# Kernel optimization log

Measured on AMD Instinct MI355X. Metric: run time of the kernel, lower is better.

## Reference

```python
import jax, jax.numpy as jnp
import numpy as np

NODE_NUM = 2048
DIM_IN = 2
DIM_OUT = 64
CHEB_K = 2
EMBED_DIM = 16
BATCH = 16


def _sagc(x, E, w_pool, b_pool):
    """AGCRN-style adaptive graph conv. x: [B,N,C]; E: [N,e];
    w_pool: [e,K,C,O]; b_pool: [e,O]. Returns (out [B,N,O], A [N,N])."""
    n = E.shape[0]
    A = E @ E.T                                   # [N,N] raw (signed) similarity
    supports = jax.nn.softmax(jax.nn.relu(A), axis=1)
    s_list = [jnp.eye(n, dtype=x.dtype), supports]
    for _ in range(2, CHEB_K):
        s_list.append(2.0 * supports @ s_list[-1] - s_list[-2])
    S = jnp.stack(s_list[:CHEB_K])                # [K,N,N]
    W = jnp.einsum('ne,ekio->nkio', E, w_pool)    # per-node weights [N,K,C,O]
    b = E @ b_pool                                # [N,O]
    x_g = jnp.einsum('knm,bmi->bnki', S, x)       # [B,N,K,C]
    out = jnp.einsum('bnki,nkio->bno', x_g, W) + b
    return out, A


def _degrees(adj_mask, H, weight):
    """adj_mask: [N,N] {0,1}; H: [B,N,D]; weight: [N,N] -> softmaxed [B,N,N]."""
    HHT = jnp.einsum('bnd,bmd->bnm', H, H)        # [B,N,N]
    AHHT = adj_mask * HHT                          # broadcast [N,N]*[B,N,N]
    AHHTW = jnp.einsum('bnm,mk->bnk', AHHT, weight)
    return jax.nn.softmax(AHHTW, axis=-1)


def setup_inputs() -> dict:
    key = jax.random.key(0)
    ks = jax.random.split(key, 9)
    din = DIM_IN + DIM_OUT
    return {
        'x': jax.random.normal(ks[0], (BATCH, NODE_NUM, DIM_IN), jnp.float32),
        'state': jax.random.normal(ks[1], (BATCH, NODE_NUM, DIM_OUT), jnp.float32),
        'node_embeddings': jax.random.normal(ks[2], (NODE_NUM, EMBED_DIM), jnp.float32) * 0.5,
        'weight_connect': jax.random.normal(ks[3], (NODE_NUM, NODE_NUM), jnp.float32) * 0.02,
        'weight_disconnect': jax.random.normal(ks[4], (NODE_NUM, NODE_NUM), jnp.float32) * 0.02,
        'gate_w': jax.random.normal(ks[5], (EMBED_DIM, CHEB_K, din, 2 * DIM_OUT), jnp.float32) * 0.05,
        'gate_b': jax.random.normal(ks[6], (EMBED_DIM, 2 * DIM_OUT), jnp.float32) * 0.05,
        'upd_w': jax.random.normal(ks[7], (EMBED_DIM, CHEB_K, din, DIM_OUT), jnp.float32) * 0.05,
        'upd_b': jax.random.normal(ks[8], (EMBED_DIM, DIM_OUT), jnp.float32) * 0.05,
    }


def reference(x, state, node_embeddings, weight_connect, weight_disconnect,
              gate_w, gate_b, upd_w, upd_b):
    inp = jnp.concatenate([x, state], axis=-1)            # [B,N,Cin+D]
    x_gconv, A = _sagc(inp, node_embeddings, gate_w, gate_b)
    z_r = jax.nn.sigmoid(x_gconv)
    z, r = jnp.split(z_r, 2, axis=-1)
    candidate = jnp.concatenate([x, z * state], axis=-1)
    hc = jnp.tanh(_sagc(candidate, node_embeddings, upd_w, upd_b)[0])
    h = r * state + (1.0 - r) * hc                        # [B,N,D]
    A_connect = jnp.where(A > 0, 1.0, 0.0).astype(h.dtype)
    A_disconnect = jnp.where(A < 0, 1.0, 0.0).astype(h.dtype)
    deg_c = _degrees(A_connect, h, weight_connect)        # [B,N,N]
    deg_d = _degrees(A_disconnect, h, weight_disconnect)
    numerator = (0.8 * h
                 - 0.1 * jnp.einsum('bnm,bmd->bnd', deg_c, h)
                 + 0.1 * jnp.einsum('bnm,bmd->bnd', deg_d, h))
    return numerator
```

## Files before the change

kernel.cpp:

```cpp
#include <hip/hip_runtime.h>
#include <hip/hip_bf16.h>

typedef unsigned short u16;
typedef unsigned int   u32;
typedef unsigned char  u8;

typedef __attribute__((ext_vector_type(8))) short bf16x8;
typedef __attribute__((ext_vector_type(4))) float f32x4;
typedef __attribute__((ext_vector_type(16))) float f32x16;

static __device__ __forceinline__ float bf2f(u16 u){ return __uint_as_float(((u32)u)<<16); }
static __device__ __forceinline__ u16 f2bf(float f){
  u32 u = __float_as_uint(f);
  u32 r = (u + 0x7fff + ((u>>16)&1)) >> 16;
  return (u16)r;
}

static __device__ __forceinline__ u8 f2fp8(float v){
  v = fminf(440.f, fmaxf(-440.f, v));
  return (u8)(__builtin_amdgcn_cvt_pk_fp8_f32(v, 0.f, 0, false) & 0xff);
}
static __device__ __forceinline__ u32 pk4_fp8(float a, float b, float c, float d){
  int w = __builtin_amdgcn_cvt_pk_fp8_f32(a, b, 0, false);
  w = __builtin_amdgcn_cvt_pk_fp8_f32(c, d, w, true);
  return (u32)w;
}

static __device__ __forceinline__ f32x4 mfma_bf16(bf16x8 a, bf16x8 b, f32x4 c){
  return __builtin_amdgcn_mfma_f32_16x16x32_bf16(a, b, c, 0, 0, 0);
}
static __device__ __forceinline__ f32x16 mfma_fp8_32(long a, long b, f32x16 c){
  return __builtin_amdgcn_mfma_f32_32x32x16_fp8_fp8(a, b, c, 0, 0, 0);
}
static __device__ __forceinline__ long lo64(uint4 v){ return (long)(((unsigned long long)v.y<<32) | v.x); }
static __device__ __forceinline__ long hi64(uint4 v){ return (long)(((unsigned long long)v.w<<32) | v.z); }
static __device__ __forceinline__ long mklong(u32 lo, u32 hi){ return (long)(((unsigned long long)hi<<32) | lo); }

__global__ void k_w8(const float* __restrict__ Wc, const float* __restrict__ Wd,
                     u8* __restrict__ Wc8, u8* __restrict__ Wd8){
  __shared__ float tile[64][65];
  const float* src = blockIdx.z ? Wd : Wc;
  u8* dst = blockIdx.z ? Wd8 : Wc8;
  const int m0 = blockIdx.x*64, k0 = blockIdx.y*64;
  const int t = threadIdx.x, r = t & 63, cc = t >> 6;
  #pragma unroll
  for (int j=0;j<4;j++){
    float4 v = *(const float4*)&src[(size_t)(m0+r)*2048 + k0 + cc*16 + j*4];
    tile[r][cc*16+j*4+0]=v.x; tile[r][cc*16+j*4+1]=v.y;
    tile[r][cc*16+j*4+2]=v.z; tile[r][cc*16+j*4+3]=v.w;
  }
  __syncthreads();
  const int lane = t & 63, sub = t >> 6;
  const int kth = sub & 1, mcp = sub >> 1;
  const int kl = kth*32 + (lane & 31);
  const int ml = mcp*32 + (lane >> 5)*8;
  u32 b0 = pk4_fp8(16.f*tile[ml+ 0][kl], 16.f*tile[ml+ 1][kl], 16.f*tile[ml+ 2][kl], 16.f*tile[ml+ 3][kl]);
  u32 b1 = pk4_fp8(16.f*tile[ml+ 4][kl], 16.f*tile[ml+ 5][kl], 16.f*tile[ml+ 6][kl], 16.f*tile[ml+ 7][kl]);
  u32 b2 = pk4_fp8(16.f*tile[ml+16][kl], 16.f*tile[ml+17][kl], 16.f*tile[ml+18][kl], 16.f*tile[ml+19][kl]);
  u32 b3 = pk4_fp8(16.f*tile[ml+20][kl], 16.f*tile[ml+21][kl], 16.f*tile[ml+22][kl], 16.f*tile[ml+23][kl]);
  const int pt = m0 >> 6, kt = (k0 >> 5) + kth;
  u8* dbase = dst + (size_t)((pt*64 + kt)*2 + mcp)*1024 + lane*16;
  *(uint4*)dbase = make_uint4(b0, b1, b2, b3);
}

__global__ void k_hcvt(const float* __restrict__ h, u16* __restrict__ hb16,
                       u8* __restrict__ ht8p, u16* __restrict__ hfm){
  __shared__ float tile[64][65];
  const int k0 = blockIdx.x*64, b = blockIdx.y;
  const int t = threadIdx.x, r = t & 63, cc = t >> 6;
  const float* src = h + ((size_t)b*2048 + k0)*64;
  u32 hw[8];
  #pragma unroll
  for (int j=0;j<4;j++){
    float4 v = *(const float4*)&src[(size_t)r*64 + cc*16 + j*4];
    tile[r][cc*16+j*4+0]=v.x; tile[r][cc*16+j*4+1]=v.y;
    tile[r][cc*16+j*4+2]=v.z; tile[r][cc*16+j*4+3]=v.w;
    hw[2*j]   = (u32)f2bf(v.x) | ((u32)f2bf(v.y)<<16);
    hw[2*j+1] = (u32)f2bf(v.z) | ((u32)f2bf(v.w)<<16);
  }
  u16* hp = hb16 + (((size_t)b*2048 + k0 + r)*64 + cc*16);
  *(uint4*)hp     = make_uint4(hw[0],hw[1],hw[2],hw[3]);
  *(uint4*)(hp+8) = make_uint4(hw[4],hw[5],hw[6],hw[7]);
  __syncthreads();
  {
    const int lane = t & 63, sub = cc;
    const int k16 = (k0 >> 4) + sub;
    const int lr = sub*16 + ((lane >> 5) << 3);
    const int d0 = lane & 31;
    #pragma unroll
    for (int dt=0; dt<2; ++dt){
      const int d = dt*32 + d0;
      u32 w0 = pk4_fp8(tile[lr+0][d], tile[lr+1][d], tile[lr+2][d], tile[lr+3][d]);
      u32 w1 = pk4_fp8(tile[lr+4][d], tile[lr+5][d], tile[lr+6][d], tile[lr+7][d]);
      *(uint2*)(ht8p + (size_t)b*131072 + (size_t)(k16*2 + dt)*512 + lane*8) = make_uint2(w0, w1);
    }
  }
  {
    const int col = k0 + r, ks = cc >> 1, q0 = (cc & 1)*2;
    const int ctg = col >> 4, lcv = col & 15;
    u16* fbase = hfm + (size_t)b*131072 + (size_t)ks*65536 + ((size_t)ctg*64)*8;
    #pragma unroll
    for (int qq=0; qq<2; ++qq){
      int q = q0 + qq;
      u32 p0 = (u32)f2bf(tile[r][ks*32+q*8+0]) | ((u32)f2bf(tile[r][ks*32+q*8+1])<<16);
      u32 p1 = (u32)f2bf(tile[r][ks*32+q*8+2]) | ((u32)f2bf(tile[r][ks*32+q*8+3])<<16);
      u32 p2 = (u32)f2bf(tile[r][ks*32+q*8+4]) | ((u32)f2bf(tile[r][ks*32+q*8+5])<<16);
      u32 p3 = (u32)f2bf(tile[r][ks*32+q*8+6]) | ((u32)f2bf(tile[r][ks*32+q*8+7])<<16);
      *(uint4*)(fbase + (size_t)(q*16 + lcv)*8) = make_uint4(p0,p1,p2,p3);
    }
  }
}

__global__ void k_P(const float* __restrict__ E, u16* __restrict__ P, u8* __restrict__ msk){
  __shared__ float Ew[16];
  __shared__ float arow[2048];
  __shared__ float red[4];
  const int t = threadIdx.x, n = blockIdx.x;
  if (t < 16) Ew[t] = E[n*16 + t];
  __syncthreads();
  float lmax = 0.f;
  for (int i=0;i<8;i++){
    int m = t + 256*i;
    const float* ep = E + m*16;
    float dot = 0.f;
    #pragma unroll
    for (int d=0; d<16; ++d) dot += Ew[d]*ep[d];
    msk[n*2048 + m] = dot > 0.f ? (u8)1 : (dot < 0.f ? (u8)2 : (u8)0);
    float ar = fmaxf(dot, 0.f);
    arow[m] = ar;
    lmax = fmaxf(lmax, ar);
  }
  for (int o=1;o<64;o<<=1) lmax = fmaxf(lmax, __shfl_xor(lmax, o));
  if ((t&63)==0) red[t>>6] = lmax;
  __syncthreads();
  float gmax = fmaxf(fmaxf(red[0],red[1]), fmaxf(red[2],red[3]));
  __syncthreads();
  float lsum = 0.f;
  for (int i=0;i<8;i++){
    int m = t + 256*i;
    float e = expf(arow[m] - gmax);
    arow[m] = e;
    lsum += e;
  }
  for (int o=1;o<64;o<<=1) lsum += __shfl_xor(lsum, o);
  if ((t&63)==0) red[t>>6] = lsum;
  __syncthreads();
  float inv = 1.f/(red[0]+red[1]+red[2]+red[3]);
  for (int i=0;i<8;i++){
    int m = t + 256*i;
    P[n*2048 + m] = f2bf(arow[m]*inv);
  }
}

__global__ void k_mbits(const u8* __restrict__ msk, u32* __restrict__ mp2, u32* __restrict__ mn2){
  const int m = blockIdx.x, nb = blockIdx.y*256;
  const int t = threadIdx.x, w = t>>6, lane = t&63;
  u8 v = msk[(size_t)(nb + t)*2048 + m];
  unsigned long long bp = __ballot(v == (u8)1);
  unsigned long long bn = __ballot(v == (u8)2);
  if (lane == 0){
    int wi = (nb + w*64) >> 5;
    mp2[(size_t)wi*2048 + m]     = (u32)bp;
    mp2[(size_t)(wi+1)*2048 + m] = (u32)(bp>>32);
    mn2[(size_t)wi*2048 + m]     = (u32)bn;
    mn2[(size_t)(wi+1)*2048 + m] = (u32)(bn>>32);
  }
}

__global__ void k_c1x(const u16* __restrict__ P, const float* __restrict__ x, float* __restrict__ c1x){
  const int t = threadIdx.x;
  const int r = t>>1, c = t&1;
  const int n = blockIdx.x*64 + r, b = blockIdx.y;
  const u16* pr = P + (size_t)n*2048;
  const float* xb = x + (size_t)b*2048*2 + c;
  float acc = 0.f;
  for (int m=0;m<2048;m+=4){
    acc += bf2f(pr[m+0])*xb[(m+0)*2];
    acc += bf2f(pr[m+1])*xb[(m+1)*2];
    acc += bf2f(pr[m+2])*xb[(m+2)*2];
    acc += bf2f(pr[m+3])*xb[(m+3)*2];
  }
  c1x[((size_t)b*2048 + n)*2 + c] = acc;
}

__global__ void k_conv(const u16* __restrict__ P, const float* __restrict__ Z, float* __restrict__ Y){
  __shared__ float Pt[16][68];
  __shared__ float Zt[16][68];
  const int t = threadIdx.x;
  const int tr = t>>4, tc = t&15;
  const int n0 = blockIdx.x*64, b = blockIdx.y;
  float acc[4][4] = {};
  for (int mt=0; mt<128; ++mt){
    int m0 = mt*16;
    {
      int r = t>>2, c4 = (t&3)*4;
      const u16* pp = P + (size_t)(n0+r)*2048 + m0 + c4;
      u32 p0 = *(const u32*)pp, p1v = *(const u32*)(pp+2);
      Pt[c4+0][r]=bf2f((u16)p0);  Pt[c4+1][r]=bf2f((u16)(p0>>16));
      Pt[c4+2][r]=bf2f((u16)p1v); Pt[c4+3][r]=bf2f((u16)(p1v>>16));
      int mm = t>>4, d0 = (t&15)*4;
      float4 zv = *(const float4*)&Z[((size_t)b*2048 + m0+mm)*64 + d0];
      Zt[mm][d0+0]=zv.x; Zt[mm][d0+1]=zv.y; Zt[mm][d0+2]=zv.z; Zt[mm][d0+3]=zv.w;
    }
    __syncthreads();
    #pragma unroll
    for (int mm=0; mm<16; ++mm){
      float4 a  = *(const float4*)&Pt[mm][tr*4];
      float4 bz = *(const float4*)&Zt[mm][tc*4];
      acc[0][0]+=a.x*bz.x; acc[0][1]+=a.x*bz.y; acc[0][2]+=a.x*bz.z; acc[0][3]+=a.x*bz.w;
      acc[1][0]+=a.y*bz.x; acc[1][1]+=a.y*bz.y; acc[1][2]+=a.y*bz.z; acc[1][3]+=a.y*bz.w;
      acc[2][0]+=a.z*bz.x; acc[2][1]+=a.z*bz.y; acc[2][2]+=a.z*bz.z; acc[2][3]+=a.z*bz.w;
      acc[3][0]+=a.w*bz.x; acc[3][1]+=a.w*bz.y; acc[3][2]+=a.w*bz.z; acc[3][3]+=a.w*bz.w;
    }
    __syncthreads();
  }
  #pragma unroll
  for (int i=0;i<4;i++){
    float4 v = make_float4(acc[i][0],acc[i][1],acc[i][2],acc[i][3]);
    *(float4*)&Y[((size_t)b*2048 + n0 + tr*4 + i)*64 + tc*4] = v;
  }
}

__global__ void k_gate(const float* __restrict__ E, const float* __restrict__ gw, const float* __restrict__ gb,
                       const float* __restrict__ x, const float* __restrict__ state,
                       const float* __restrict__ c1x, const float* __restrict__ c1s,
                       float* __restrict__ zs, float* __restrict__ rws){
  __shared__ float Ew[16];
  __shared__ float bnv[128];
  __shared__ float Wn[2][66][64];
  __shared__ float xg4[4][2][66];
  const int t = threadIdx.x, n = blockIdx.x;
  if (t < 16) Ew[t] = E[n*16 + t];
  __syncthreads();
  if (t < 128){
    float a = 0.f;
    #pragma unroll
    for (int e=0;e<16;e++) a += Ew[e]*gb[e*128 + t];
    bnv[t] = a;
  }
  for (int half=0; half<2; ++half){
    for (int idx=t; idx<8448; idx+=256){
      int o = idx & 63, rest = idx>>6, i = rest % 66, k = rest / 66;
      float a = 0.f;
      #pragma unroll
      for (int e=0;e<16;e++) a += Ew[e]*gw[((e*2+k)*66 + i)*128 + half*64 + o];
      Wn[k][i][o] = a;
    }
    __syncthreads();
    for (int bb=0; bb<4; ++bb){
      for (int idx=t; idx<528; idx+=256){
        int bi = idx/132, rem = idx%132, k = rem/66, i = rem%66;
        int b = bb*4 + bi;
        float v;
        if (k==0) v = (i<2) ? x[((size_t)b*2048+n)*2 + i] : state[((size_t)b*2048+n)*64 + (i-2)];
        else      v = (i<2) ? c1x[((size_t)b*2048+n)*2 + i] : c1s[((size_t)b*2048+n)*64 + (i-2)];
        xg4[bi][k][i] = v;
      }
      __syncthreads();
      {
        int bi = t>>6, o = t&63, b = bb*4 + bi;
        float a = 0.f;
        #pragma unroll
        for (int k=0;k<2;k++)
          for (int i=0;i<66;i++) a += xg4[bi][k][i]*Wn[k][i][o];
        a += bnv[half*64 + o];
        float s = 1.f/(1.f + expf(-a));
        if (half==0) zs[((size_t)b*2048+n)*64 + o] = s*state[((size_t)b*2048+n)*64 + o];
        else         rws[((size_t)b*2048+n)*64 + o] = s;
      }
      __syncthreads();
    }
  }
}

__global__ void k_upd(const float* __restrict__ E, const float* __restrict__ uw, const float* __restrict__ ub,
                      const float* __restrict__ x, const float* __restrict__ state,
                      const float* __restrict__ zs, const float* __restrict__ c1x, const float* __restrict__ c2s,
                      const float* __restrict__ rws, float* __restrict__ h){
  __shared__ float Ew[16];
  __shared__ float bnu[64];
  __shared__ float Wn[2][66][64];
  __shared__ float xg4[4][2][66];
  const int t = threadIdx.x, n = blockIdx.x;
  if (t < 16) Ew[t] = E[n*16 + t];
  __syncthreads();
  if (t < 64){
    float a = 0.f;
    #pragma unroll
    for (int e=0;e<16;e++) a += Ew[e]*ub[e*64 + t];
    bnu[t] = a;
  }
  for (int idx=t; idx<8448; idx+=256){
    int o = idx & 63, rest = idx>>6, i = rest % 66, k = rest / 66;
    float a = 0.f;
    #pragma unroll
    for (int e=0;e<16;e++) a += Ew[e]*uw[((e*2+k)*66 + i)*64 + o];
    Wn[k][i][o] = a;
  }
  __syncthreads();
  for (int bb=0; bb<4; ++bb){
    for (int idx=t; idx<528; idx+=256){
      int bi = idx/132, rem = idx%132, k = rem/66, i = rem%66;
      int b = bb*4 + bi;
      float v;
      if (k==0) v = (i<2) ? x[((size_t)b*2048+n)*2 + i] : zs[((size_t)b*2048+n)*64 + (i-2)];
      else      v = (i<2) ? c1x[((size_t)b*2048+n)*2 + i] : c2s[((size_t)b*2048+n)*64 + (i-2)];
      xg4[bi][k][i] = v;
    }
    __syncthreads();
    {
      int bi = t>>6, o = t&63, b = bb*4 + bi;
      float a = 0.f;
      #pragma unroll
      for (int k=0;k<2;k++)
        for (int i=0;i<66;i++) a += xg4[bi][k][i]*Wn[k][i][o];
      float hc = tanhf(a + bnu[o]);
      float rv = rws[((size_t)b*2048+n)*64 + o];
      h[((size_t)b*2048+n)*64 + o] = rv*state[((size_t)b*2048+n)*64 + o] + (1.f - rv)*hc;
    }
    __syncthreads();
  }
}

#define SROW8 2056

__global__ void __launch_bounds__(512,2) k_deg(
    const u32* __restrict__ mbits, const u16* __restrict__ hb16,
    const u8* __restrict__ W8,
    const u8* __restrict__ ht8p, const u16* __restrict__ hfm,
    const float* __restrict__ hf32, const float* __restrict__ oc_in,
    float* __restrict__ outp, int fin){
  extern __shared__ u8 S[];
  __shared__ float maxw[64][4];
  __shared__ float sumw[64][4];
  __shared__ float sgl_lds[64];
  const int t = threadIdx.x;
  const int w = t >> 6, lane = t & 63, lc = lane & 15, q = lane >> 4;
  const int l32 = lane & 31, h32 = lane >> 5;
  const int id = blockIdx.x;
  const int b = id >> 5, n0 = (id & 31) * 64;
  const int p0 = (id >> 3) & 31;
  const u32* mrow0 = mbits + (size_t)(n0 >> 5)*2048;
  const u32* mrow1 = mrow0 + 2048;
  const u16* hbb = hb16 + (size_t)b*2048*64;
  const u16* hfb = hfm + (size_t)b*131072;
  const u8* htb = ht8p + (size_t)b*131072;

  {
    const int c0 = p0 & 15;
    bf16x8 A[4][2];
    #pragma unroll
    for (int rt=0; rt<4; ++rt)
      #pragma unroll
      for (int ks=0; ks<2; ++ks)
        A[rt][ks] = *(const bf16x8*)&hbb[(size_t)(n0 + rt*16 + lc)*64 + ks*32 + q*8];
    int ctg0 = w*16 + c0;
    bf16x8 B0c = *(const bf16x8*)(hfb + (size_t)ctg0*512 + lane*8);
    bf16x8 B1c = *(const bf16x8*)(hfb + 65536 + (size_t)ctg0*512 + lane*8);
    u32 m0c = mrow0[ctg0*16 + lc], m1c = mrow1[ctg0*16 + lc];
    #pragma unroll 1
    for (int ct=0; ct<16; ++ct){
      const int ctg  = w*16 + ((ct + c0) & 15);
      const int ctgn = w*16 + ((ct + 1 + c0) & 15);
      bf16x8 B0n = *(const bf16x8*)(hfb + (size_t)ctgn*512 + lane*8);
      bf16x8 B1n = *(const bf16x8*)(hfb + 65536 + (size_t)ctgn*512 + lane*8);
      u32 m0n = mrow0[ctgn*16 + lc], m1n = mrow1[ctgn*16 + lc];
      const int mcol = ctg*16 + lc;
      f32x4 a[4];
      #pragma unroll
      for (int rt=0; rt<4; ++rt){
        a[rt] = (f32x4){0.f,0.f,0.f,0.f};
        a[rt] = mfma_bf16(A[rt][0], B0c, a[rt]);
        a[rt] = mfma_bf16(A[rt][1], B1c, a[rt]);
      }
      #pragma unroll
      for (int rt=0; rt<4; ++rt){
        const u32 mw = (rt < 2) ? m0c : m1c;
        #pragma unroll
        for (int i=0;i<4;i++){
          const int row = rt*16 + q*4 + i;
          float v = ((mw >> (row & 31)) & 1u) ? a[rt][i]*0.125f : 0.f;
          S[row*SROW8 + mcol] = f2fp8(v);
        }
      }
      B0c = B0n; B1c = B1n; m0c = m0n; m1c = m1n;
    }
  }
  __syncthreads();

  const int nh = w >> 2, kq = w & 3;
  const u8* sbase = S + (size_t)(nh*32 + l32)*SROW8 + h32*8;
  const u8* wl = W8 + lane*16;
  f32x16 o0 = (f32x16)(0.f), o1 = (f32x16)(0.f);
  float mrun = -1e30f, srun = 0.f;
  const float LN256 = 5.545177444479562f;
  #pragma unroll 1
  for (int si = 0; si < 4; ++si){
    const int ktb = kq*16 + si*4;
    f32x16 L[4];
    #pragma unroll
    for (int tt=0; tt<4; ++tt) L[tt] = (f32x16)(0.f);
    uint4 wv[8];
    {
      const int pt0 = p0 & 31;
      #pragma unroll
      for (int tt=0; tt<4; ++tt){
        wv[tt*2+0] = *(const uint4*)(wl + (size_t)(((pt0*64 + ktb+tt)*2 + 0))*1024);
        wv[tt*2+1] = *(const uint4*)(wl + (size_t)(((pt0*64 + ktb+tt)*2 + 1))*1024);
      }
    }
    __builtin_amdgcn_s_setprio(1);
    #pragma unroll 1
    for (int pti = 0; pti < 32; ++pti){
      const int pt  = (pti + p0) & 31;
      const int ptn = (pti + 1 + p0) & 31;
      long b0 = *(const long*)(sbase + pt*64 +  0);
      long b1 = *(const long*)(sbase + pt*64 + 16);
      long b2 = *(const long*)(sbase + pt*64 + 32);
      long b3 = *(const long*)(sbase + pt*64 + 48);
      uint4 wn[8];
      #pragma unroll
      for (int tt=0; tt<4; ++tt){
        wn[tt*2+0] = *(const uint4*)(wl + (size_t)(((ptn*64 + ktb+tt)*2 + 0))*1024);
        wn[tt*2+1] = *(const uint4*)(wl + (size_t)(((ptn*64 + ktb+tt)*2 + 1))*1024);
      }
      #pragma unroll
      for (int tt=0; tt<4; ++tt) L[tt] = mfma_fp8_32(lo64(wv[tt*2+0]), b0, L[tt]);
      #pragma unroll
      for (int tt=0; tt<4; ++tt) L[tt] = mfma_fp8_32(hi64(wv[tt*2+0]), b1, L[tt]);
      #pragma unroll
      for (int tt=0; tt<4; ++tt) L[tt] = mfma_fp8_32(lo64(wv[tt*2+1]), b2, L[tt]);
      #pragma unroll
      for (int tt=0; tt<4; ++tt) L[tt] = mfma_fp8_32(hi64(wv[tt*2+1]), b3, L[tt]);
      #pragma unroll
      for (int i=0; i<8; ++i) wv[i] = wn[i];
    }
    __builtin_amdgcn_s_setprio(0);
    float cmax = L[0][0];
    #pragma unroll
    for (int tt=0; tt<4; ++tt)
      #pragma unroll
      for (int g=0; g<16; ++g) cmax = fmaxf(cmax, L[tt][g]);
    cmax = fmaxf(cmax, __shfl_xor(cmax, 32));
    float mnew = fmaxf(mrun, 0.5f*cmax);
    float sc = __expf(mrun - mnew);
    srun *= sc;
    #pragma unroll
    for (int g=0; g<16; ++g){
      const int rowl = (g&3) + 8*(g>>2) + 4*h32;
      float fr = __shfl(sc, rowl);
      o0[g] *= fr; o1[g] *= fr;
    }
    float cs = 0.f;
    #pragma unroll
    for (int tt=0; tt<4; ++tt){
      float p[16];
      #pragma unroll
      for (int g=0; g<16; ++g){
        p[g] = __expf(0.5f*L[tt][g] - mnew + LN256);
        cs += p[g];
      }
      u32 qA = pk4_fp8(p[0],p[1],p[2],p[3]);
      u32 qB = pk4_fp8(p[4],p[5],p[6],p[7]);
      u32 qC = pk4_fp8(p[8],p[9],p[10],p[11]);
      u32 qD = pk4_fp8(p[12],p[13],p[14],p[15]);
      u32 xA = __shfl_xor(qA, 32), xB = __shfl_xor(qB, 32);
      u32 xC = __shfl_xor(qC, 32), xD = __shfl_xor(qD, 32);
      long pf0 = h32 ? mklong(xB, qB) : mklong(qA, xA);
      long pf1 = h32 ? mklong(xD, qD) : mklong(qC, xC);
      const int kt = ktb + tt;
      long h00 = *(const long*)(htb + (size_t)((kt*2+0)*2 + 0)*512 + lane*8);
      long h01 = *(const long*)(htb + (size_t)((kt*2+0)*2 + 1)*512 + lane*8);
      long h10 = *(const long*)(htb + (size_t)((kt*2+1)*2 + 0)*512 + lane*8);
      long h11 = *(const long*)(htb + (size_t)((kt*2+1)*2 + 1)*512 + lane*8);
      o0 = mfma_fp8_32(pf0, h00, o0);
      o1 = mfma_fp8_32(pf0, h01, o1);
      o0 = mfma_fp8_32(pf1, h10, o0);
      o1 = mfma_fp8_32(pf1, h11, o1);
    }
    cs += __shfl_xor(cs, 32);
    srun += cs;
    mrun = mnew;
  }

  if (lane < 32){
    maxw[nh*32 + lane][kq] = mrun;
    sumw[nh*32 + lane][kq] = srun;
  }
  __syncthreads();
  {
    float m_gl = maxw[nh*32 + l32][0];
    #pragma unroll
    for (int j=1;j<4;j++) m_gl = fmaxf(m_gl, maxw[nh*32 + l32][j]);
    float s_gl = 0.f;
    #pragma unroll
    for (int j=0;j<4;j++) s_gl += sumw[nh*32 + l32][j] * __expf(maxw[nh*32 + l32][j] - m_gl);
    if (kq == 0 && lane < 32) sgl_lds[nh*32 + lane] = s_gl;
    float f = __expf(mrun - m_gl);
    float* scr = (float*)S;
    #pragma unroll
    for (int g=0; g<16; ++g){
      const int rowl = (g&3) + 8*(g>>2) + 4*h32;
      float fr = __shfl(f, rowl);
      scr[(size_t)(kq*2 + nh)*2048 + (size_t)g*64 + lane]      = o0[g]*fr;
      scr[(size_t)(kq*2 + nh)*2048 + (size_t)(16+g)*64 + lane] = o1[g]*fr;
    }
  }
  __syncthreads();

  {
    const float* scr = (const float*)S;
    const int n_g = t >> 3, d0 = (t & 7)*8;
    const int nh_r = n_g >> 5, nl = n_g & 31;
    const int h32r = (nl >> 2) & 1;
    const int rr = nl - 4*h32r;
    const int g = (rr & 3) | ((rr >> 3) << 2);
    const float sdiv = sgl_lds[n_g];
    float* op = outp + (size_t)b*2048*64;
    const float* hp = hf32 + (size_t)b*2048*64;
    const float* cp = oc_in + (size_t)b*2048*64;
    #pragma unroll
    for (int j=0;j<8;j++){
      const int d = d0 + j;
      const int dt = d >> 5;
      const int lanei = (d & 31) + 32*h32r;
      float v = 0.f;
      #pragma unroll
      for (int kqr=0; kqr<4; ++kqr)
        v += scr[(size_t)(kqr*2 + nh_r)*2048 + (size_t)(dt*16 + g)*64 + lanei];
      v /= sdiv;
      size_t idx = (size_t)(n0 + n_g)*64 + d;
      if (fin) v = 0.8f*hp[idx] - 0.1f*cp[idx] + 0.1f*v;
      op[idx] = v;
    }
  }
}

extern "C" void kernel_launch(void* const* d_in, const int* in_sizes, int n_in,
                              void* d_out, int out_size, void* d_ws, size_t ws_size,
                              hipStream_t stream) {
  const float* x     = (const float*)d_in[0];
  const float* state = (const float*)d_in[1];
  const float* E     = (const float*)d_in[2];
  const float* Wc    = (const float*)d_in[3];
  const float* Wd    = (const float*)d_in[4];
  const float* gw    = (const float*)d_in[5];
  const float* gb    = (const float*)d_in[6];
  const float* uw    = (const float*)d_in[7];
  const float* ub    = (const float*)d_in[8];

  char* base = (char*)d_ws;
  u16*   P    = (u16*)(base + 0);
  u32*   mp2  = (u32*)(base + 0);
  u32*   mn2  = (u32*)(base + 524288);
  u8*    msk  = (u8*) (base + 8388608);
  u8*    Wc8  = (u8*) (base + 12582912);
  u8*    Wd8  = (u8*) (base + 16777216);
  u16*   hb16 = (u16*)(base + 20971520);
  u8*    ht8p = (u8*) (base + 25165824);
  u16*   hfm  = (u16*)(base + 27262976);
  float* c1x  = (float*)(base + 31457280);
  float* c1s  = (float*)(base + 31719424);
  float* zs   = (float*)(base + 40108032);
  float* rws  = (float*)(base + 48496640);
  float* c2s  = (float*)(base + 56885248);
  float* h    = (float*)(base + 65273856);
  float* oc   = c1s;
  float* od   = c2s;

  k_w8<<<dim3(32,32,2), 256, 0, stream>>>(Wc, Wd, Wc8, Wd8);
  k_P<<<2048, 256, 0, stream>>>(E, P, msk);
  k_c1x<<<dim3(32,16), 128, 0, stream>>>(P, x, c1x);
  k_conv<<<dim3(32,16), 256, 0, stream>>>(P, state, c1s);
  k_gate<<<2048, 256, 0, stream>>>(E, gw, gb, x, state, c1x, c1s, zs, rws);
  k_conv<<<dim3(32,16), 256, 0, stream>>>(P, zs, c2s);
  k_upd<<<2048, 256, 0, stream>>>(E, uw, ub, x, state, zs, c1x, c2s, rws, h);
  k_hcvt<<<dim3(32,16), 256, 0, stream>>>(h, hb16, ht8p, hfm);
  k_mbits<<<dim3(2048,8), 256, 0, stream>>>(msk, mp2, mn2);

  const int deg_lds = 64*SROW8;
  hipFuncSetAttribute((const void*)k_deg, hipFuncAttributeMaxDynamicSharedMemorySize, deg_lds);
  k_deg<<<512, 512, deg_lds, stream>>>(mp2, hb16, Wc8, ht8p, hfm, h, h, oc, 0);
  k_deg<<<512, 512, deg_lds, stream>>>(mn2, hb16, Wd8, ht8p, hfm, h, oc, (float*)d_out, 1);
}
```

Baseline: 1.232 ms.

## Use MFMA with split-bf16 in k_conv and repartition k_deg warps over K

k_conv now uses 32x32x16 bf16 MFMA instead of a scalar FP32 outer-product loop. It keeps accuracy by splitting Z into high and low bf16 parts and summing two accumulators. In k_deg, each of the 8 warps now covers both 32-row halves of the 64-node tile over its own K slice, instead of the old 2x4 node-half by K-quarter split. This lets each weight fragment loaded from global memory feed two MFMAs, halving W8 traffic per warp. The cost is more accumulator registers per warp and an 8-way reduction of softmax partials and outputs through LDS.

```diff
diff --git a/kernel.cpp b/kernel.cpp
--- a/kernel.cpp
+++ b/kernel.cpp
@@ -28,6 +28,9 @@
 
 static __device__ __forceinline__ f32x4 mfma_bf16(bf16x8 a, bf16x8 b, f32x4 c){
   return __builtin_amdgcn_mfma_f32_16x16x32_bf16(a, b, c, 0, 0, 0);
+}
+static __device__ __forceinline__ f32x16 mfma_bf16_32(bf16x8 a, bf16x8 b, f32x16 c){
+  return __builtin_amdgcn_mfma_f32_32x32x16_bf16(a, b, c, 0, 0, 0);
 }
 static __device__ __forceinline__ f32x16 mfma_fp8_32(long a, long b, f32x16 c){
   return __builtin_amdgcn_mfma_f32_32x32x16_fp8_fp8(a, b, c, 0, 0, 0);
@@ -184,40 +187,49 @@
 }
 
 __global__ void k_conv(const u16* __restrict__ P, const float* __restrict__ Z, float* __restrict__ Y){
-  __shared__ float Pt[16][68];
-  __shared__ float Zt[16][68];
+  __shared__ u16 Pt[64][68];
+  __shared__ u16 Zhi[64][68];
+  __shared__ u16 Zlo[64][68];
   const int t = threadIdx.x;
-  const int tr = t>>4, tc = t&15;
+  const int w = t >> 6, lane = t & 63, l32 = lane & 31, h32 = lane >> 5;
+  const int nh = w & 1, dh = w >> 1;
   const int n0 = blockIdx.x*64, b = blockIdx.y;
-  float acc[4][4] = {};
-  for (int mt=0; mt<128; ++mt){
-    int m0 = mt*16;
+  const int mloc = t & 63, grp = t >> 6;
+  f32x16 acch = (f32x16)(0.f), accl = (f32x16)(0.f);
+  for (int mc = 0; mc < 32; ++mc){
+    const int m0 = mc*64;
     {
-      int r = t>>2, c4 = (t&3)*4;
-      const u16* pp = P + (size_t)(n0+r)*2048 + m0 + c4;
-      u32 p0 = *(const u32*)pp, p1v = *(const u32*)(pp+2);
-      Pt[c4+0][r]=bf2f((u16)p0);  Pt[c4+1][r]=bf2f((u16)(p0>>16));
-      Pt[c4+2][r]=bf2f((u16)p1v); Pt[c4+3][r]=bf2f((u16)(p1v>>16));
-      int mm = t>>4, d0 = (t&15)*4;
-      float4 zv = *(const float4*)&Z[((size_t)b*2048 + m0+mm)*64 + d0];
-      Zt[mm][d0+0]=zv.x; Zt[mm][d0+1]=zv.y; Zt[mm][d0+2]=zv.z; Zt[mm][d0+3]=zv.w;
+      const u16* pp = P + (size_t)(n0 + mloc)*2048 + m0 + grp*16;
+      uint4 v0 = *(const uint4*)pp;
+      uint4 v1 = *(const uint4*)(pp + 8);
+      *(uint4*)&Pt[mloc][grp*16]     = v0;
+      *(uint4*)&Pt[mloc][grp*16 + 8] = v1;
+      const float* zp = Z + ((size_t)b*2048 + m0 + mloc)*64 + grp*16;
+      #pragma unroll
+      for (int jj = 0; jj < 4; ++jj){
+        float4 zv = *(const float4*)(zp + jj*4);
+        const int dd = grp*16 + jj*4;
+        u16 h0 = f2bf(zv.x); Zhi[dd+0][mloc] = h0; Zlo[dd+0][mloc] = f2bf(zv.x - bf2f(h0));
+        u16 h1 = f2bf(zv.y); Zhi[dd+1][mloc] = h1; Zlo[dd+1][mloc] = f2bf(zv.y - bf2f(h1));
+        u16 h2 = f2bf(zv.z); Zhi[dd+2][mloc] = h2; Zlo[dd+2][mloc] = f2bf(zv.z - bf2f(h2));
+        u16 h3 = f2bf(zv.w); Zhi[dd+3][mloc] = h3; Zlo[dd+3][mloc] = f2bf(zv.w - bf2f(h3));
+      }
     }
     __syncthreads();
     #pragma unroll
-    for (int mm=0; mm<16; ++mm){
-      float4 a  = *(const float4*)&Pt[mm][tr*4];
-      float4 bz = *(const float4*)&Zt[mm][tc*4];
-      acc[0][0]+=a.x*bz.x; acc[0][1]+=a.x*bz.y; acc[0][2]+=a.x*bz.z; acc[0][3]+=a.x*bz.w;
-      acc[1][0]+=a.y*bz.x; acc[1][1]+=a.y*bz.y; acc[1][2]+=a.y*bz.z; acc[1][3]+=a.y*bz.w;
-      acc[2][0]+=a.z*bz.x; acc[2][1]+=a.z*bz.y; acc[2][2]+=a.z*bz.z; acc[2][3]+=a.z*bz.w;
-      acc[3][0]+=a.w*bz.x; acc[3][1]+=a.w*bz.y; acc[3][2]+=a.w*bz.z; acc[3][3]+=a.w*bz.w;
+    for (int kt = 0; kt < 4; ++kt){
+      bf16x8 a  = *(const bf16x8*)&Pt[nh*32 + l32][kt*16 + h32*8];
+      bf16x8 bh = *(const bf16x8*)&Zhi[dh*32 + l32][kt*16 + h32*8];
+      bf16x8 bl = *(const bf16x8*)&Zlo[dh*32 + l32][kt*16 + h32*8];
+      acch = mfma_bf16_32(a, bh, acch);
+      accl = mfma_bf16_32(a, bl, accl);
     }
     __syncthreads();
   }
   #pragma unroll
-  for (int i=0;i<4;i++){
-    float4 v = make_float4(acc[i][0],acc[i][1],acc[i][2],acc[i][3]);
-    *(float4*)&Y[((size_t)b*2048 + n0 + tr*4 + i)*64 + tc*4] = v;
+  for (int g = 0; g < 16; ++g){
+    const int row = (g&3) + 8*(g>>2) + 4*h32;
+    Y[((size_t)b*2048 + n0 + nh*32 + row)*64 + dh*32 + l32] = acch[g] + accl[g];
   }
 }
 
@@ -322,6 +334,58 @@
   }
 }
 
+static __device__ __forceinline__ void sm_step(f32x16& LK0, f32x16& LK1,
+    f32x16& OA, f32x16& OB, float& mrun, float& srun,
+    const u8* __restrict__ htb, int ktA, int ktB, int lane, int h32){
+  const float LN256 = 5.545177444479562f;
+  float cmax = LK0[0];
+  #pragma unroll
+  for (int g=1; g<16; ++g) cmax = fmaxf(cmax, LK0[g]);
+  #pragma unroll
+  for (int g=0; g<16; ++g) cmax = fmaxf(cmax, LK1[g]);
+  cmax = fmaxf(cmax, __shfl_xor(cmax, 32));
+  float mnew = fmaxf(mrun, 0.5f*cmax);
+  float sc = __expf(mrun - mnew);
+  srun *= sc;
+  #pragma unroll
+  for (int g=0; g<16; ++g){
+    const int rowl = (g&3) + 8*(g>>2) + 4*h32;
+    float fr = __shfl(sc, rowl);
+    OA[g] *= fr; OB[g] *= fr;
+  }
+  float cs = 0.f;
+  #pragma unroll
+  for (int kti=0; kti<2; ++kti){
+    const int kt = kti ? ktB : ktA;
+    float p[16];
+    #pragma unroll
+    for (int g=0; g<16; ++g){
+      float Lg = kti ? LK1[g] : LK0[g];
+      p[g] = __expf(0.5f*Lg - mnew + LN256);
+      cs += p[g];
+    }
+    u32 qA = pk4_fp8(p[0],p[1],p[2],p[3]);
+    u32 qB = pk4_fp8(p[4],p[5],p[6],p[7]);
+    u32 qC = pk4_fp8(p[8],p[9],p[10],p[11]);
+    u32 qD = pk4_fp8(p[12],p[13],p[14],p[15]);
+    u32 xA = __shfl_xor(qA,32), xB = __shfl_xor(qB,32);
+    u32 xC = __shfl_xor(qC,32), xD = __shfl_xor(qD,32);
+    long pf0 = h32 ? mklong(xB,qB) : mklong(qA,xA);
+    long pf1 = h32 ? mklong(xD,qD) : mklong(qC,xC);
+    long h00 = *(const long*)(htb + (size_t)((kt*2+0)*2 + 0)*512 + lane*8);
+    long h01 = *(const long*)(htb + (size_t)((kt*2+0)*2 + 1)*512 + lane*8);
+    long h10 = *(const long*)(htb + (size_t)((kt*2+1)*2 + 0)*512 + lane*8);
+    long h11 = *(const long*)(htb + (size_t)((kt*2+1)*2 + 1)*512 + lane*8);
+    OA = mfma_fp8_32(pf0, h00, OA);
+    OB = mfma_fp8_32(pf0, h01, OB);
+    OA = mfma_fp8_32(pf1, h10, OA);
+    OB = mfma_fp8_32(pf1, h11, OB);
+  }
+  cs += __shfl_xor(cs, 32);
+  srun += cs;
+  mrun = mnew;
+}
+
 #define SROW8 2056
 
 __global__ void __launch_bounds__(512,2) k_deg(
@@ -331,8 +395,8 @@
     const float* __restrict__ hf32, const float* __restrict__ oc_in,
     float* __restrict__ outp, int fin){
   extern __shared__ u8 S[];
-  __shared__ float maxw[64][4];
-  __shared__ float sumw[64][4];
+  __shared__ float maxw[64][8];
+  __shared__ float sumw[64][8];
   __shared__ float sgl_lds[64];
   const int t = threadIdx.x;
   const int w = t >> 6, lane = t & 63, lc = lane & 15, q = lane >> 4;
@@ -388,133 +452,105 @@
   }
   __syncthreads();
 
-  const int nh = w >> 2, kq = w & 3;
-  const u8* sbase = S + (size_t)(nh*32 + l32)*SROW8 + h32*8;
+  const u8* sb0 = S + (size_t)l32*SROW8 + h32*8;
+  const u8* sb1 = S + (size_t)(32 + l32)*SROW8 + h32*8;
   const u8* wl = W8 + lane*16;
-  f32x16 o0 = (f32x16)(0.f), o1 = (f32x16)(0.f);
-  float mrun = -1e30f, srun = 0.f;
-  const float LN256 = 5.545177444479562f;
+  f32x16 oA0 = (f32x16)(0.f), oA1 = (f32x16)(0.f);
+  f32x16 oB0 = (f32x16)(0.f), oB1 = (f32x16)(0.f);
+  float mrun0 = -1e30f, srun0 = 0.f, mrun1 = -1e30f, srun1 = 0.f;
   #pragma unroll 1
   for (int si = 0; si < 4; ++si){
-    const int ktb = kq*16 + si*4;
-    f32x16 L[4];
-    #pragma unroll
-    for (int tt=0; tt<4; ++tt) L[tt] = (f32x16)(0.f);
-    uint4 wv[8];
+    const int ktA = w*8 + si*2, ktB = ktA + 1;
+    f32x16 L00 = (f32x16)(0.f), L01 = (f32x16)(0.f);
+    f32x16 L10 = (f32x16)(0.f), L11 = (f32x16)(0.f);
+    uint4 wv0, wv1, wv2, wv3;
     {
-      const int pt0 = p0 & 31;
-      #pragma unroll
-      for (int tt=0; tt<4; ++tt){
-        wv[tt*2+0] = *(const uint4*)(wl + (size_t)(((pt0*64 + ktb+tt)*2 + 0))*1024);
-        wv[tt*2+1] = *(const uint4*)(wl + (size_t)(((pt0*64 + ktb+tt)*2 + 1))*1024);
-      }
+      const int pt0 = p0;
+      wv0 = *(const uint4*)(wl + (size_t)((pt0*64 + ktA)*2 + 0)*1024);
+      wv1 = *(const uint4*)(wl + (size_t)((pt0*64 + ktA)*2 + 1)*1024);
+      wv2 = *(const uint4*)(wl + (size_t)((pt0*64 + ktB)*2 + 0)*1024);
+      wv3 = *(const uint4*)(wl + (size_t)((pt0*64 + ktB)*2 + 1)*1024);
     }
     __builtin_amdgcn_s_setprio(1);
     #pragma unroll 1
     for (int pti = 0; pti < 32; ++pti){
       const int pt  = (pti + p0) & 31;
       const int ptn = (pti + 1 + p0) & 31;
-      long b0 = *(const long*)(sbase + pt*64 +  0);
-      long b1 = *(const long*)(sbase + pt*64 + 16);
-      long b2 = *(const long*)(sbase + pt*64 + 32);
-      long b3 = *(const long*)(sbase + pt*64 + 48);
-      uint4 wn[8];
-      #pragma unroll
-      for (int tt=0; tt<4; ++tt){
-        wn[tt*2+0] = *(const uint4*)(wl + (size_t)(((ptn*64 + ktb+tt)*2 + 0))*1024);
-        wn[tt*2+1] = *(const uint4*)(wl + (size_t)(((ptn*64 + ktb+tt)*2 + 1))*1024);
-      }
-      #pragma unroll
-      for (int tt=0; tt<4; ++tt) L[tt] = mfma_fp8_32(lo64(wv[tt*2+0]), b0, L[tt]);
-      #pragma unroll
-      for (int tt=0; tt<4; ++tt) L[tt] = mfma_fp8_32(hi64(wv[tt*2+0]), b1, L[tt]);
-      #pragma unroll
-      for (int tt=0; tt<4; ++tt) L[tt] = mfma_fp8_32(lo64(wv[tt*2+1]), b2, L[tt]);
-      #pragma unroll
-      for (int tt=0; tt<4; ++tt) L[tt] = mfma_fp8_32(hi64(wv[tt*2+1]), b3, L[tt]);
-      #pragma unroll
-      for (int i=0; i<8; ++i) wv[i] = wn[i];
+      long b00 = *(const long*)(sb0 + pt*64 +  0);
+      long b01 = *(const long*)(sb0 + pt*64 + 16);
+      long b02 = *(const long*)(sb0 + pt*64 + 32);
+      long b03 = *(const long*)(sb0 + pt*64 + 48);
+      long b10 = *(const long*)(sb1 + pt*64 +  0);
+      long b11 = *(const long*)(sb1 + pt*64 + 16);
+      long b12 = *(const long*)(sb1 + pt*64 + 32);
+      long b13 = *(const long*)(sb1 + pt*64 + 48);
+      uint4 wn0 = *(const uint4*)(wl + (size_t)((ptn*64 + ktA)*2 + 0)*1024);
+      uint4 wn1 = *(const uint4*)(wl + (size_t)((ptn*64 + ktA)*2 + 1)*1024);
+      uint4 wn2 = *(const uint4*)(wl + (size_t)((ptn*64 + ktB)*2 + 0)*1024);
+      uint4 wn3 = *(const uint4*)(wl + (size_t)((ptn*64 + ktB)*2 + 1)*1024);
+      L00 = mfma_fp8_32(lo64(wv0), b00, L00);
+      L01 = mfma_fp8_32(lo64(wv0), b10, L01);
+      L10 = mfma_fp8_32(lo64(wv2), b00, L10);
+      L11 = mfma_fp8_32(lo64(wv2), b10, L11);
+      L00 = mfma_fp8_32(hi64(wv0), b01, L00);
+      L01 = mfma_fp8_32(hi64(wv0), b11, L01);
+      L10 = mfma_fp8_32(hi64(wv2), b01, L10);
+      L11 = mfma_fp8_32(hi64(wv2), b11, L11);
+      L00 = mfma_fp8_32(lo64(wv1), b02, L00);
+      L01 = mfma_fp8_32(lo64(wv1), b12, L01);
+      L10 = mfma_fp8_32(lo64(wv3), b02, L10);
+      L11 = mfma_fp8_32(lo64(wv3), b12, L11);
+      L00 = mfma_fp8_32(hi64(wv1), b03, L00);
+      L01 = mfma_fp8_32(hi64(wv1), b13, L01);
+      L10 = mfma_fp8_32(hi64(wv3), b03, L10);
+      L11 = mfma_fp8_32(hi64(wv3), b13, L11);
+      wv0 = wn0; wv1 = wn1; wv2 = wn2; wv3 = wn3;
     }
     __builtin_amdgcn_s_setprio(0);
-    float cmax = L[0][0];
-    #pragma unroll
-    for (int tt=0; tt<4; ++tt)
-      #pragma unroll
-      for (int g=0; g<16; ++g) cmax = fmaxf(cmax, L[tt][g]);
-    cmax = fmaxf(cmax, __shfl_xor(cmax, 32));
-    float mnew = fmaxf(mrun, 0.5f*cmax);
-    float sc = __expf(mrun - mnew);
-    srun *= sc;
+    sm_step(L00, L10, oA0, oA1, mrun0, srun0, htb, ktA, ktB, lane, h32);
+    sm_step(L01, L11, oB0, oB1, mrun1, srun1, htb, ktA, ktB, lane, h32);
+  }
+
+  if (h32 == 0){
+    maxw[l32][w] = mrun0;      sumw[l32][w] = srun0;
+    maxw[32 + l32][w] = mrun1; sumw[32 + l32][w] = srun1;
+  }
+  __syncthreads();
+  float* scr = (float*)S;
+  {
+    float m_g0 = maxw[l32][0];
+    #pragma unroll
+    for (int j=1;j<8;j++) m_g0 = fmaxf(m_g0, maxw[l32][j]);
+    float s_g0 = 0.f;
+    #pragma unroll
+    for (int j=0;j<8;j++) s_g0 += sumw[l32][j]*__expf(maxw[l32][j]-m_g0);
+    float m_g1 = maxw[32+l32][0];
+    #pragma unroll
+    for (int j=1;j<8;j++) m_g1 = fmaxf(m_g1, maxw[32+l32][j]);
+    float s_g1 = 0.f;
+    #pragma unroll
+    for (int j=0;j<8;j++) s_g1 += sumw[32+l32][j]*__expf(maxw[32+l32][j]-m_g1);
+    if (w == 0 && h32 == 0){
+      sgl_lds[l32] = s_g0;
+      sgl_lds[32 + l32] = s_g1;
+    }
+    float f0 = __expf(mrun0 - m_g0);
+    float f1 = __expf(mrun1 - m_g1);
     #pragma unroll
     for (int g=0; g<16; ++g){
       const int rowl = (g&3) + 8*(g>>2) + 4*h32;
-      float fr = __shfl(sc, rowl);
-      o0[g] *= fr; o1[g] *= fr;
-    }
-    float cs = 0.f;
-    #pragma unroll
-    for (int tt=0; tt<4; ++tt){
-      float p[16];
-      #pragma unroll
-      for (int g=0; g<16; ++g){
-        p[g] = __expf(0.5f*L[tt][g] - mnew + LN256);
-        cs += p[g];
-      }
-      u32 qA = pk4_fp8(p[0],p[1],p[2],p[3]);
-      u32 qB = pk4_fp8(p[4],p[5],p[6],p[7]);
-      u32 qC = pk4_fp8(p[8],p[9],p[10],p[11]);
-      u32 qD = pk4_fp8(p[12],p[13],p[14],p[15]);
-      u32 xA = __shfl_xor(qA, 32), xB = __shfl_xor(qB, 32);
-      u32 xC = __shfl_xor(qC, 32), xD = __shfl_xor(qD, 32);
-      long pf0 = h32 ? mklong(xB, qB) : mklong(qA, xA);
-      long pf1 = h32 ? mklong(xD, qD) : mklong(qC, xC);
-      const int kt = ktb + tt;
-      long h00 = *(const long*)(htb + (size_t)((kt*2+0)*2 + 0)*512 + lane*8);
-      long h01 = *(const long*)(htb + (size_t)((kt*2+0)*2 + 1)*512 + lane*8);
-      long h10 = *(const long*)(htb + (size_t)((kt*2+1)*2 + 0)*512 + lane*8);
-      long h11 = *(const long*)(htb + (size_t)((kt*2+1)*2 + 1)*512 + lane*8);
-      o0 = mfma_fp8_32(pf0, h00, o0);
-      o1 = mfma_fp8_32(pf0, h01, o1);
-      o0 = mfma_fp8_32(pf1, h10, o0);
-      o1 = mfma_fp8_32(pf1, h11, o1);
-    }
-    cs += __shfl_xor(cs, 32);
-    srun += cs;
-    mrun = mnew;
-  }
-
-  if (lane < 32){
-    maxw[nh*32 + lane][kq] = mrun;
-    sumw[nh*32 + lane][kq] = srun;
-  }
-  __syncthreads();
+      float fr0 = __shfl(f0, rowl);
+      float fr1 = __shfl(f1, rowl);
+      scr[((size_t)w*64 + rowl)*64 + l32]           = oA0[g]*fr0;
+      scr[((size_t)w*64 + rowl)*64 + 32 + l32]      = oA1[g]*fr0;
+      scr[((size_t)w*64 + 32 + rowl)*64 + l32]      = oB0[g]*fr1;
+      scr[((size_t)w*64 + 32 + rowl)*64 + 32 + l32] = oB1[g]*fr1;
+    }
+  }
+  __syncthreads();
+
   {
-    float m_gl = maxw[nh*32 + l32][0];
-    #pragma unroll
-    for (int j=1;j<4;j++) m_gl = fmaxf(m_gl, maxw[nh*32 + l32][j]);
-    float s_gl = 0.f;
-    #pragma unroll
-    for (int j=0;j<4;j++) s_gl += sumw[nh*32 + l32][j] * __expf(maxw[nh*32 + l32][j] - m_gl);
-    if (kq == 0 && lane < 32) sgl_lds[nh*32 + lane] = s_gl;
-    float f = __expf(mrun - m_gl);
-    float* scr = (float*)S;
-    #pragma unroll
-    for (int g=0; g<16; ++g){
-      const int rowl = (g&3) + 8*(g>>2) + 4*h32;
-      float fr = __shfl(f, rowl);
-      scr[(size_t)(kq*2 + nh)*2048 + (size_t)g*64 + lane]      = o0[g]*fr;
-      scr[(size_t)(kq*2 + nh)*2048 + (size_t)(16+g)*64 + lane] = o1[g]*fr;
-    }
-  }
-  __syncthreads();
-
-  {
-    const float* scr = (const float*)S;
     const int n_g = t >> 3, d0 = (t & 7)*8;
-    const int nh_r = n_g >> 5, nl = n_g & 31;
-    const int h32r = (nl >> 2) & 1;
-    const int rr = nl - 4*h32r;
-    const int g = (rr & 3) | ((rr >> 3) << 2);
     const float sdiv = sgl_lds[n_g];
     float* op = outp + (size_t)b*2048*64;
     const float* hp = hf32 + (size_t)b*2048*64;
@@ -522,12 +558,10 @@
     #pragma unroll
     for (int j=0;j<8;j++){
       const int d = d0 + j;
-      const int dt = d >> 5;
-      const int lanei = (d & 31) + 32*h32r;
       float v = 0.f;
       #pragma unroll
-      for (int kqr=0; kqr<4; ++kqr)
-        v += scr[(size_t)(kqr*2 + nh_r)*2048 + (size_t)(dt*16 + g)*64 + lanei];
+      for (int qq=0; qq<8; ++qq)
+        v += scr[((size_t)qq*64 + n_g)*64 + d];
       v /= sdiv;
       size_t idx = (size_t)(n0 + n_g)*64 + d;
       if (fin) v = 0.8f*hp[idx] - 0.1f*cp[idx] + 0.1f*v;
```

After: 1.029 ms. 1.2x faster.
